# Performance work log

Measured on AMD Instinct MI355X. Metric: run time of the kernel, lower is better.

Reference implementation:

```python
import jax, jax.numpy as jnp
import numpy as np

B, N, E = 128, 2000, 2000
EMBED, HIDDEN = 256, 512


def setup_inputs() -> dict:
    key = jax.random.key(0)
    k1, k2, k3, k4, k5, k6, k7 = jax.random.split(key, 7)
    node_embeddings = jax.random.normal(k1, (B, N, EMBED), dtype=jnp.float32)
    locs = jax.random.uniform(k2, (B, N, 2), dtype=jnp.float32)
    edge_list = jax.random.randint(k3, (B, E, 2), 0, N, dtype=jnp.int64)
    in_dim = 2 * EMBED + 1
    # Kaiming-ish init for the two Linear layers of edge_scorer
    W1 = jax.random.normal(k4, (in_dim, HIDDEN), dtype=jnp.float32) / np.sqrt(in_dim)
    b1 = jnp.zeros((HIDDEN,), dtype=jnp.float32)
    W2 = jax.random.normal(k5, (HIDDEN, 1), dtype=jnp.float32) / np.sqrt(HIDDEN)
    b2 = jnp.zeros((1,), dtype=jnp.float32)
    return {
        "node_embeddings": node_embeddings,
        "locs": locs,
        "edge_list": edge_list,
        "delete_bias": 0,
        "W1": W1,
        "b1": b1,
        "W2": W2,
        "b2": b2,
    }


def reference(node_embeddings, locs, edge_list, delete_bias, W1, b1, W2, b2):
    # valid mask for -1-padded edges
    valid = (edge_list[..., 0] >= 0) & (edge_list[..., 1] >= 0)  # (B, E)
    edges = jnp.clip(edge_list, 0, None)
    bidx = jnp.arange(node_embeddings.shape[0])[:, None]  # (B, 1)
    i, j = edges[..., 0], edges[..., 1]  # (B, E)
    emb_i = node_embeddings[bidx, i]  # (B, E, D)
    emb_j = node_embeddings[bidx, j]  # (B, E, D)
    d = locs[bidx, i] - locs[bidx, j]  # (B, E, 2)
    dist = jnp.sqrt(jnp.sum(d * d, axis=-1, keepdims=True))  # (B, E, 1)
    feats = jnp.concatenate([emb_i, emb_j, dist], axis=-1)  # (B, E, 2D+1)
    h = jax.nn.relu(jnp.einsum('bef,fh->beh', feats, W1) + b1)
    logits = (jnp.einsum('beh,ho->beo', h, W2) + b2)[..., 0]  # (B, E)
    logits = jnp.where(valid, logits, -jnp.inf)
    return logits + jnp.float32(delete_bias)
```

## Files before the change

### kernel.cpp

```cpp
#include <hip/hip_runtime.h>
#include <math.h>

#define EMBED    256
#define HIDDEN   512
#define Nn       2000
#define Ee       2000
#define BM       128
#define TILES    8
#define NBLK     250
#define NTHREADS 512
#define FP       264

typedef __attribute__((ext_vector_type(8)))  short bf16x8;
typedef __attribute__((ext_vector_type(16))) float f32x16;

static __device__ __forceinline__ short f2bf(float f) {
  unsigned u = __builtin_bit_cast(unsigned, f);
  u += 0x7fffu + ((u >> 16) & 1u);
  return (short)(u >> 16);
}

static __device__ __forceinline__ bf16x8 cvt8(float4 a, float4 b) {
  bf16x8 v;
  v[0]=f2bf(a.x); v[1]=f2bf(a.y); v[2]=f2bf(a.z); v[3]=f2bf(a.w);
  v[4]=f2bf(b.x); v[5]=f2bf(b.y); v[6]=f2bf(b.z); v[7]=f2bf(b.w);
  return v;
}

#define LBAR() do { asm volatile("s_waitcnt lgkmcnt(0)" ::: "memory"); \
                    __builtin_amdgcn_s_barrier(); \
                    asm volatile("" ::: "memory"); } while (0)

__global__ void w1f_kernel(const float* __restrict__ W1, short* __restrict__ W1F) {
  const int t  = blockIdx.x * 512 + threadIdx.x;
  const int l  = t & 63;
  const int tk = (t >> 6) & 31;
  const int tn = t >> 11;
  const int n  = tn * 32 + (l & 31);
  const int k0 = tk * 16 + (l >> 5) * 8;
  bf16x8 v;
#pragma unroll
  for (int q = 0; q < 8; ++q)
    v[q] = f2bf(W1[(size_t)(k0 + q) * HIDDEN + n]);
  *(bf16x8*)(W1F + (size_t)t * 8) = v;
}

__global__ __launch_bounds__(NTHREADS, 2)
void edge_kernel(const float* __restrict__ emb, const float* __restrict__ locs,
                 const int* __restrict__ edges, const int* __restrict__ dbias,
                 const float* __restrict__ W1, const float* __restrict__ b1,
                 const float* __restrict__ W2, const float* __restrict__ b2,
                 const short* __restrict__ W1F, float* __restrict__ out)
{
  __shared__ short feat[2][BM][FP];
  __shared__ float b1_s[HIDDEN], w513_s[HIDDEN], w2_s[HIDDEN];
  __shared__ float part_s[8][BM];
  __shared__ float dist_s[2][BM];
  __shared__ int   valid_s[2][BM];
  __shared__ int   ibase_s[2][BM], jbase_s[2][BM];

  const int tid = threadIdx.x;

  const int orig = blockIdx.x;
  const int xcd  = orig & 7;
  const int idx  = orig >> 3;
  const int sbid = (xcd < 2 ? xcd * 32 : 64 + (xcd - 2) * 31) + idx;
  const int eblk = sbid * (TILES * BM);

  b1_s[tid]   = b1[tid];
  w513_s[tid] = W1[(size_t)512 * HIDDEN + tid];
  w2_s[tid]   = W2[tid];
  const float b2s_base = b2[0] + (float)dbias[0];

  auto do_meta = [&](int T) {
    const int g  = eblk + T * BM + tid;
    const int b  = g / Ee;
    const int i0 = edges[2 * g];
    const int j0 = edges[2 * g + 1];
    valid_s[T & 1][tid] = (i0 >= 0) && (j0 >= 0);
    const int ib = b * Nn + (i0 < 0 ? 0 : i0);
    const int jb = b * Nn + (j0 < 0 ? 0 : j0);
    ibase_s[T & 1][tid] = ib;
    jbase_s[T & 1][tid] = jb;
    const float dx = locs[2 * (size_t)ib]     - locs[2 * (size_t)jb];
    const float dy = locs[2 * (size_t)ib + 1] - locs[2 * (size_t)jb + 1];
    dist_s[T & 1][tid] = sqrtf(dx * dx + dy * dy);
  };

  if (tid < BM) do_meta(0);
  LBAR();

  const int sq = tid & 7;
  const int eh = tid >> 3;
  const int lane = tid & 63;
  const int w    = tid >> 6;
  const int ln31 = lane & 31;
  const int kg   = lane >> 5;

#pragma unroll
  for (int r = 0; r < 2; ++r) {
    const int el = r * 64 + eh;
    const float* src = emb + (size_t)ibase_s[0][el] * EMBED + sq * 8;
#pragma unroll
    for (int m = 0; m < 4; ++m) {
      float4 a  = *(const float4*)(src + m * 64);
      float4 b4 = *(const float4*)(src + m * 64 + 4);
      *(bf16x8*)&feat[0][el][(sq + 8 * m) * 8] = cvt8(a, b4);
    }
  }
  LBAR();

  f32x16 acc[4][2];
#pragma unroll
  for (int et = 0; et < 4; ++et)
#pragma unroll
    for (int nt = 0; nt < 2; ++nt)
#pragma unroll
      for (int q = 0; q < 16; ++q) acc[et][nt][q] = 0.f;

  const short* wfb = W1F + (size_t)(w * 2 * 32) * 512 + lane * 8;

#pragma unroll 1
  for (int p = 0; p < 2 * TILES; ++p) {
    const int bb   = p & 1;
    const int nbuf = bb ^ 1;
    const int half = p & 1;
    const int tps  = (p + 1) >> 1;
    const int sh   = (p + 1) & 1;
    const bool stg = p < 2 * TILES - 1;

    bf16x8 wc0 = *(const bf16x8*)(wfb + (size_t)(half * 16) * 512);
    bf16x8 wc1 = *(const bf16x8*)(wfb + (size_t)(32 + half * 16) * 512);

    float4 hg00, hg01, hg10, hg11;

#pragma unroll
    for (int ks = 0; ks < 16; ++ks) {
      bf16x8 wn0, wn1;
      if (ks < 15) {
        wn0 = *(const bf16x8*)(wfb + (size_t)(half * 16 + ks + 1) * 512);
        wn1 = *(const bf16x8*)(wfb + (size_t)(32 + half * 16 + ks + 1) * 512);
      }

      if (stg && (ks & 3) == 0) {
        const int g2 = ks >> 2;
        const int el = (g2 >> 1) * 64 + eh;
        const int rb = sh ? jbase_s[tps & 1][el] : ibase_s[tps & 1][el];
        const float* src = emb + (size_t)rb * EMBED + sq * 8 + (g2 & 1) * 128;
        hg00 = *(const float4*)(src);
        hg01 = *(const float4*)(src + 4);
        hg10 = *(const float4*)(src + 64);
        hg11 = *(const float4*)(src + 68);
      }
      if (stg && (ks & 3) == 3) {
        const int g2 = ks >> 2;
        const int el = (g2 >> 1) * 64 + eh;
        const int mb = (g2 & 1) * 2;
        *(bf16x8*)&feat[nbuf][el][(sq + 8 * mb) * 8]       = cvt8(hg00, hg01);
        *(bf16x8*)&feat[nbuf][el][(sq + 8 * (mb + 1)) * 8] = cvt8(hg10, hg11);
      }
      if ((p & 1) == 0 && ks == 1 && tid < BM && (p >> 1) + 1 < TILES)
        do_meta((p >> 1) + 1);

#pragma unroll
      for (int et = 0; et < 4; ++et) {
        bf16x8 fb = *(const bf16x8*)(&feat[bb][et * 32 + ln31][ks * 16 + kg * 8]);
        acc[et][0] = __builtin_amdgcn_mfma_f32_32x32x16_bf16(wc0, fb, acc[et][0], 0, 0, 0);
        acc[et][1] = __builtin_amdgcn_mfma_f32_32x32x16_bf16(wc1, fb, acc[et][1], 0, 0, 0);
      }
      wc0 = wn0; wc1 = wn1;
    }
    LBAR();

    if (p & 1) {
      const int t   = p >> 1;
      const int mb2 = t & 1;
      float dv[4], ps[4];
#pragma unroll
      for (int et = 0; et < 4; ++et) {
        dv[et] = dist_s[mb2][et * 32 + ln31];
        ps[et] = 0.f;
      }
#pragma unroll
      for (int nt = 0; nt < 2; ++nt) {
#pragma unroll
        for (int r = 0; r < 16; ++r) {
          const int n = w * 64 + nt * 32 + (r & 3) + ((r >> 2) << 3) + (kg << 2);
          const float bias = b1_s[n];
          const float wd   = w513_s[n];
          const float w2v  = w2_s[n];
#pragma unroll
          for (int et = 0; et < 4; ++et) {
            float pv = acc[et][nt][r] + bias + dv[et] * wd;
            ps[et] += fmaxf(pv, 0.f) * w2v;
          }
        }
      }
#pragma unroll
      for (int et = 0; et < 4; ++et) ps[et] += __shfl_xor(ps[et], 32, 64);
      if (lane < 32) {
#pragma unroll
        for (int et = 0; et < 4; ++et) part_s[w][et * 32 + ln31] = ps[et];
      }
      LBAR();
      if (tid < BM) {
        float s = 0.f;
#pragma unroll
        for (int wv = 0; wv < 8; ++wv) s += part_s[wv][tid];
        float logit = s + b2s_base;
        if (!valid_s[mb2][tid]) logit = -__builtin_inff();
        out[eblk + t * BM + tid] = logit;
      }
#pragma unroll
      for (int et = 0; et < 4; ++et)
#pragma unroll
        for (int nt = 0; nt < 2; ++nt)
#pragma unroll
          for (int q = 0; q < 16; ++q) acc[et][nt][q] = 0.f;
    }
  }
}

extern "C" void kernel_launch(void* const* d_in, const int* in_sizes, int n_in,
                              void* d_out, int out_size, void* d_ws, size_t ws_size,
                              hipStream_t stream) {
  const float* emb   = (const float*)d_in[0];
  const float* locs  = (const float*)d_in[1];
  const int*   edges = (const int*)d_in[2];
  const int*   dbias = (const int*)d_in[3];
  const float* W1    = (const float*)d_in[4];
  const float* b1    = (const float*)d_in[5];
  const float* W2    = (const float*)d_in[6];
  const float* b2    = (const float*)d_in[7];
  float*       out   = (float*)d_out;
  short*       W1F   = (short*)d_ws;

  w1f_kernel<<<dim3(64), dim3(512), 0, stream>>>(W1, W1F);
  edge_kernel<<<dim3(NBLK), dim3(NTHREADS), 0, stream>>>(
      emb, locs, edges, dbias, W1, b1, W2, b2, (const short*)W1F, out);
}
```

Measured before the change: 151.7 us.

## Repartition waves to 2 edge-halves by 4 hidden-groups and raise MFMA priority

The warp tiling changes from each wave covering all 128 edges by 64 hidden units to each wave covering 64 edges by 128 hidden units. Per k-step each wave now reads 2 feature fragments from LDS instead of 4, but loads 4 W1 fragments from global/L2 instead of 2. The goal is less LDS traffic per MFMA, at the cost of more global weight loads and extra weight registers. The MFMA block is also wrapped in s_setprio, and the cross-wave reduction is adjusted to the new layout.

```diff
diff --git a/kernel.cpp b/kernel.cpp
--- a/kernel.cpp
+++ b/kernel.cpp
@@ -54,7 +54,7 @@
 {
   __shared__ short feat[2][BM][FP];
   __shared__ float b1_s[HIDDEN], w513_s[HIDDEN], w2_s[HIDDEN];
-  __shared__ float part_s[8][BM];
+  __shared__ float part_s[8][64];
   __shared__ float dist_s[2][BM];
   __shared__ int   valid_s[2][BM];
   __shared__ int   ibase_s[2][BM], jbase_s[2][BM];
@@ -91,15 +91,17 @@
   LBAR();
 
   const int sq = tid & 7;
-  const int eh = tid >> 3;
+  const int ehs = tid >> 3;
   const int lane = tid & 63;
   const int w    = tid >> 6;
+  const int eh   = w & 1;
+  const int ng   = w >> 1;
   const int ln31 = lane & 31;
   const int kg   = lane >> 5;
 
 #pragma unroll
   for (int r = 0; r < 2; ++r) {
-    const int el = r * 64 + eh;
+    const int el = r * 64 + ehs;
     const float* src = emb + (size_t)ibase_s[0][el] * EMBED + sq * 8;
 #pragma unroll
     for (int m = 0; m < 4; ++m) {
@@ -110,15 +112,15 @@
   }
   LBAR();
 
-  f32x16 acc[4][2];
-#pragma unroll
-  for (int et = 0; et < 4; ++et)
-#pragma unroll
-    for (int nt = 0; nt < 2; ++nt)
+  f32x16 acc[2][4];
+#pragma unroll
+  for (int et = 0; et < 2; ++et)
+#pragma unroll
+    for (int nt = 0; nt < 4; ++nt)
 #pragma unroll
       for (int q = 0; q < 16; ++q) acc[et][nt][q] = 0.f;
 
-  const short* wfb = W1F + (size_t)(w * 2 * 32) * 512 + lane * 8;
+  const short* wfb = W1F + (size_t)(ng * 4 * 32) * 512 + lane * 8;
 
 #pragma unroll 1
   for (int p = 0; p < 2 * TILES; ++p) {
@@ -129,22 +131,24 @@
     const int sh   = (p + 1) & 1;
     const bool stg = p < 2 * TILES - 1;
 
-    bf16x8 wc0 = *(const bf16x8*)(wfb + (size_t)(half * 16) * 512);
-    bf16x8 wc1 = *(const bf16x8*)(wfb + (size_t)(32 + half * 16) * 512);
+    bf16x8 wc[4], wn[4];
+#pragma unroll
+    for (int nt = 0; nt < 4; ++nt)
+      wc[nt] = *(const bf16x8*)(wfb + (size_t)(nt * 32 + half * 16) * 512);
 
     float4 hg00, hg01, hg10, hg11;
 
 #pragma unroll
     for (int ks = 0; ks < 16; ++ks) {
-      bf16x8 wn0, wn1;
       if (ks < 15) {
-        wn0 = *(const bf16x8*)(wfb + (size_t)(half * 16 + ks + 1) * 512);
-        wn1 = *(const bf16x8*)(wfb + (size_t)(32 + half * 16 + ks + 1) * 512);
+#pragma unroll
+        for (int nt = 0; nt < 4; ++nt)
+          wn[nt] = *(const bf16x8*)(wfb + (size_t)(nt * 32 + half * 16 + ks + 1) * 512);
       }
 
       if (stg && (ks & 3) == 0) {
         const int g2 = ks >> 2;
-        const int el = (g2 >> 1) * 64 + eh;
+        const int el = (g2 >> 1) * 64 + ehs;
         const int rb = sh ? jbase_s[tps & 1][el] : ibase_s[tps & 1][el];
         const float* src = emb + (size_t)rb * EMBED + sq * 8 + (g2 & 1) * 128;
         hg00 = *(const float4*)(src);
@@ -154,7 +158,7 @@
       }
       if (stg && (ks & 3) == 3) {
         const int g2 = ks >> 2;
-        const int el = (g2 >> 1) * 64 + eh;
+        const int el = (g2 >> 1) * 64 + ehs;
         const int mb = (g2 & 1) * 2;
         *(bf16x8*)&feat[nbuf][el][(sq + 8 * mb) * 8]       = cvt8(hg00, hg01);
         *(bf16x8*)&feat[nbuf][el][(sq + 8 * (mb + 1)) * 8] = cvt8(hg10, hg11);
@@ -162,59 +166,65 @@
       if ((p & 1) == 0 && ks == 1 && tid < BM && (p >> 1) + 1 < TILES)
         do_meta((p >> 1) + 1);
 
-#pragma unroll
-      for (int et = 0; et < 4; ++et) {
-        bf16x8 fb = *(const bf16x8*)(&feat[bb][et * 32 + ln31][ks * 16 + kg * 8]);
-        acc[et][0] = __builtin_amdgcn_mfma_f32_32x32x16_bf16(wc0, fb, acc[et][0], 0, 0, 0);
-        acc[et][1] = __builtin_amdgcn_mfma_f32_32x32x16_bf16(wc1, fb, acc[et][1], 0, 0, 0);
-      }
-      wc0 = wn0; wc1 = wn1;
+      bf16x8 fb0 = *(const bf16x8*)(&feat[bb][eh * 64 + ln31][ks * 16 + kg * 8]);
+      bf16x8 fb1 = *(const bf16x8*)(&feat[bb][eh * 64 + 32 + ln31][ks * 16 + kg * 8]);
+
+      __builtin_amdgcn_s_setprio(1);
+#pragma unroll
+      for (int nt = 0; nt < 4; ++nt) {
+        acc[0][nt] = __builtin_amdgcn_mfma_f32_32x32x16_bf16(wc[nt], fb0, acc[0][nt], 0, 0, 0);
+        acc[1][nt] = __builtin_amdgcn_mfma_f32_32x32x16_bf16(wc[nt], fb1, acc[1][nt], 0, 0, 0);
+      }
+      __builtin_amdgcn_s_setprio(0);
+#pragma unroll
+      for (int nt = 0; nt < 4; ++nt) wc[nt] = wn[nt];
     }
     LBAR();
 
     if (p & 1) {
       const int t   = p >> 1;
       const int mb2 = t & 1;
-      float dv[4], ps[4];
-#pragma unroll
-      for (int et = 0; et < 4; ++et) {
-        dv[et] = dist_s[mb2][et * 32 + ln31];
+      float dv[2], ps[2];
+#pragma unroll
+      for (int et = 0; et < 2; ++et) {
+        dv[et] = dist_s[mb2][eh * 64 + et * 32 + ln31];
         ps[et] = 0.f;
       }
 #pragma unroll
-      for (int nt = 0; nt < 2; ++nt) {
+      for (int nt = 0; nt < 4; ++nt) {
 #pragma unroll
         for (int r = 0; r < 16; ++r) {
-          const int n = w * 64 + nt * 32 + (r & 3) + ((r >> 2) << 3) + (kg << 2);
+          const int n = ng * 128 + nt * 32 + (r & 3) + ((r >> 2) << 3) + (kg << 2);
           const float bias = b1_s[n];
           const float wd   = w513_s[n];
           const float w2v  = w2_s[n];
 #pragma unroll
-          for (int et = 0; et < 4; ++et) {
+          for (int et = 0; et < 2; ++et) {
             float pv = acc[et][nt][r] + bias + dv[et] * wd;
             ps[et] += fmaxf(pv, 0.f) * w2v;
           }
         }
       }
 #pragma unroll
-      for (int et = 0; et < 4; ++et) ps[et] += __shfl_xor(ps[et], 32, 64);
+      for (int et = 0; et < 2; ++et) ps[et] += __shfl_xor(ps[et], 32, 64);
       if (lane < 32) {
 #pragma unroll
-        for (int et = 0; et < 4; ++et) part_s[w][et * 32 + ln31] = ps[et];
+        for (int et = 0; et < 2; ++et) part_s[w][et * 32 + ln31] = ps[et];
       }
       LBAR();
       if (tid < BM) {
-        float s = 0.f;
-#pragma unroll
-        for (int wv = 0; wv < 8; ++wv) s += part_s[wv][tid];
+        const int ehh = tid >> 6;
+        const int es  = tid & 63;
+        float s = part_s[ehh][es] + part_s[2 + ehh][es] +
+                  part_s[4 + ehh][es] + part_s[6 + ehh][es];
         float logit = s + b2s_base;
         if (!valid_s[mb2][tid]) logit = -__builtin_inff();
         out[eblk + t * BM + tid] = logit;
       }
 #pragma unroll
-      for (int et = 0; et < 4; ++et)
-#pragma unroll
-        for (int nt = 0; nt < 2; ++nt)
+      for (int et = 0; et < 2; ++et)
+#pragma unroll
+        for (int nt = 0; nt < 4; ++nt)
 #pragma unroll
           for (int q = 0; q < 16; ++q) acc[et][nt][q] = 0.f;
     }
```

Result: slower. 162.8 us (+7.3%).

## Split edge kernel into producer and MFMA waves with smaller edge tiles

Applied to the files above, without the earlier changes.

Restructures the edge kernel around warp specialization. Four waves only issue MFMAs with raised priority and run the bias/ReLU/W2 epilogue. The other four waves gather and convert the next embedding tile, compute edge metadata and write the logits of the previous tile. The edge tile shrinks from 128 to 64 with twice as many tiles, and each MFMA wave now covers 256 hidden units for 32 edges. The goal is to hide gather latency behind compute and drop the extra in-loop barrier. The trade-off is half as many waves issuing MFMAs, and W1 fragments are now loaded from global memory inside the inner loop without the old register prefetch.

```diff
diff --git a/kernel.cpp b/kernel.cpp
--- a/kernel.cpp
+++ b/kernel.cpp
@@ -5,8 +5,8 @@
 #define HIDDEN   512
 #define Nn       2000
 #define Ee       2000
-#define BM       128
-#define TILES    8
+#define BM       64
+#define TILES    16
 #define NBLK     250
 #define NTHREADS 512
 #define FP       264
@@ -54,7 +54,7 @@
 {
   __shared__ short feat[2][BM][FP];
   __shared__ float b1_s[HIDDEN], w513_s[HIDDEN], w2_s[HIDDEN];
-  __shared__ float part_s[8][BM];
+  __shared__ float part_s[2][2][BM];
   __shared__ float dist_s[2][BM];
   __shared__ int   valid_s[2][BM];
   __shared__ int   ibase_s[2][BM], jbase_s[2][BM];
@@ -72,152 +72,121 @@
   w2_s[tid]   = W2[tid];
   const float b2s_base = b2[0] + (float)dbias[0];
 
-  auto do_meta = [&](int T) {
-    const int g  = eblk + T * BM + tid;
-    const int b  = g / Ee;
-    const int i0 = edges[2 * g];
-    const int j0 = edges[2 * g + 1];
-    valid_s[T & 1][tid] = (i0 >= 0) && (j0 >= 0);
-    const int ib = b * Nn + (i0 < 0 ? 0 : i0);
-    const int jb = b * Nn + (j0 < 0 ? 0 : j0);
-    ibase_s[T & 1][tid] = ib;
-    jbase_s[T & 1][tid] = jb;
-    const float dx = locs[2 * (size_t)ib]     - locs[2 * (size_t)jb];
-    const float dy = locs[2 * (size_t)ib + 1] - locs[2 * (size_t)jb + 1];
-    dist_s[T & 1][tid] = sqrtf(dx * dx + dy * dy);
-  };
-
-  if (tid < BM) do_meta(0);
-  LBAR();
-
-  const int sq = tid & 7;
-  const int eh = tid >> 3;
   const int lane = tid & 63;
   const int w    = tid >> 6;
   const int ln31 = lane & 31;
   const int kg   = lane >> 5;
 
-#pragma unroll
-  for (int r = 0; r < 2; ++r) {
-    const int el = r * 64 + eh;
-    const float* src = emb + (size_t)ibase_s[0][el] * EMBED + sq * 8;
-#pragma unroll
-    for (int m = 0; m < 4; ++m) {
-      float4 a  = *(const float4*)(src + m * 64);
-      float4 b4 = *(const float4*)(src + m * 64 + 4);
-      *(bf16x8*)&feat[0][el][(sq + 8 * m) * 8] = cvt8(a, b4);
+  const int pt  = tid - 256;
+  const int sq  = pt & 7;
+  const int ehs = (pt >> 3) & 31;
+
+  auto do_meta = [&](int T) {
+    const int g  = eblk + T * BM + pt;
+    const int b  = g / Ee;
+    const int i0 = edges[2 * g];
+    const int j0 = edges[2 * g + 1];
+    valid_s[T & 1][pt] = (i0 >= 0) && (j0 >= 0);
+    const int ib = b * Nn + (i0 < 0 ? 0 : i0);
+    const int jb = b * Nn + (j0 < 0 ? 0 : j0);
+    ibase_s[T & 1][pt] = ib;
+    jbase_s[T & 1][pt] = jb;
+    const float dx = locs[2 * (size_t)ib]     - locs[2 * (size_t)jb];
+    const float dy = locs[2 * (size_t)ib + 1] - locs[2 * (size_t)jb + 1];
+    dist_s[T & 1][pt] = sqrtf(dx * dx + dy * dy);
+  };
+
+  auto stage = [&](int tps, int sh, int dst) {
+#pragma unroll
+    for (int r = 0; r < 2; ++r) {
+      const int el = r * 32 + ehs;
+      const int rb = sh ? jbase_s[tps & 1][el] : ibase_s[tps & 1][el];
+      const float* src = emb + (size_t)rb * EMBED + sq * 8;
+#pragma unroll
+      for (int m = 0; m < 4; ++m) {
+        float4 a  = *(const float4*)(src + m * 64);
+        float4 b4 = *(const float4*)(src + m * 64 + 4);
+        *(bf16x8*)&feat[dst][el][(sq + 8 * m) * 8] = cvt8(a, b4);
+      }
     }
-  }
+  };
+
+  if (w == 4) do_meta(0);
   LBAR();
-
-  f32x16 acc[4][2];
-#pragma unroll
-  for (int et = 0; et < 4; ++et)
-#pragma unroll
-    for (int nt = 0; nt < 2; ++nt)
-#pragma unroll
-      for (int q = 0; q < 16; ++q) acc[et][nt][q] = 0.f;
-
-  const short* wfb = W1F + (size_t)(w * 2 * 32) * 512 + lane * 8;
+  if (w >= 4) stage(0, 0, 0);
+  LBAR();
+
+  const int eh = w & 1;
+  const int ng = w >> 1;
+
+  f32x16 acc[8];
+#pragma unroll
+  for (int nt = 0; nt < 8; ++nt)
+#pragma unroll
+    for (int q = 0; q < 16; ++q) acc[nt][q] = 0.f;
+
+  const short* wfb = W1F + (size_t)(ng * 8 * 32) * 512 + lane * 8;
 
 #pragma unroll 1
   for (int p = 0; p < 2 * TILES; ++p) {
     const int bb   = p & 1;
-    const int nbuf = bb ^ 1;
     const int half = p & 1;
-    const int tps  = (p + 1) >> 1;
-    const int sh   = (p + 1) & 1;
-    const bool stg = p < 2 * TILES - 1;
-
-    bf16x8 wc0 = *(const bf16x8*)(wfb + (size_t)(half * 16) * 512);
-    bf16x8 wc1 = *(const bf16x8*)(wfb + (size_t)(32 + half * 16) * 512);
-
-    float4 hg00, hg01, hg10, hg11;
-
-#pragma unroll
-    for (int ks = 0; ks < 16; ++ks) {
-      bf16x8 wn0, wn1;
-      if (ks < 15) {
-        wn0 = *(const bf16x8*)(wfb + (size_t)(half * 16 + ks + 1) * 512);
-        wn1 = *(const bf16x8*)(wfb + (size_t)(32 + half * 16 + ks + 1) * 512);
-      }
-
-      if (stg && (ks & 3) == 0) {
-        const int g2 = ks >> 2;
-        const int el = (g2 >> 1) * 64 + eh;
-        const int rb = sh ? jbase_s[tps & 1][el] : ibase_s[tps & 1][el];
-        const float* src = emb + (size_t)rb * EMBED + sq * 8 + (g2 & 1) * 128;
-        hg00 = *(const float4*)(src);
-        hg01 = *(const float4*)(src + 4);
-        hg10 = *(const float4*)(src + 64);
-        hg11 = *(const float4*)(src + 68);
-      }
-      if (stg && (ks & 3) == 3) {
-        const int g2 = ks >> 2;
-        const int el = (g2 >> 1) * 64 + eh;
-        const int mb = (g2 & 1) * 2;
-        *(bf16x8*)&feat[nbuf][el][(sq + 8 * mb) * 8]       = cvt8(hg00, hg01);
-        *(bf16x8*)&feat[nbuf][el][(sq + 8 * (mb + 1)) * 8] = cvt8(hg10, hg11);
-      }
-      if ((p & 1) == 0 && ks == 1 && tid < BM && (p >> 1) + 1 < TILES)
-        do_meta((p >> 1) + 1);
-
-#pragma unroll
-      for (int et = 0; et < 4; ++et) {
-        bf16x8 fb = *(const bf16x8*)(&feat[bb][et * 32 + ln31][ks * 16 + kg * 8]);
-        acc[et][0] = __builtin_amdgcn_mfma_f32_32x32x16_bf16(wc0, fb, acc[et][0], 0, 0, 0);
-        acc[et][1] = __builtin_amdgcn_mfma_f32_32x32x16_bf16(wc1, fb, acc[et][1], 0, 0, 0);
-      }
-      wc0 = wn0; wc1 = wn1;
+
+    if (w < 4) {
+      __builtin_amdgcn_s_setprio(1);
+#pragma unroll
+      for (int ks = 0; ks < 16; ++ks) {
+        bf16x8 fb = *(const bf16x8*)(&feat[bb][eh * 32 + ln31][ks * 16 + kg * 8]);
+#pragma unroll
+        for (int nt = 0; nt < 8; ++nt) {
+          bf16x8 wa = *(const bf16x8*)(wfb + (size_t)(nt * 32 + half * 16 + ks) * 512);
+          acc[nt] = __builtin_amdgcn_mfma_f32_32x32x16_bf16(wa, fb, acc[nt], 0, 0, 0);
+        }
+      }
+      __builtin_amdgcn_s_setprio(0);
+
+      if (p & 1) {
+        const int t   = p >> 1;
+        const int par = t & 1;
+        const float dv = dist_s[par][eh * 32 + ln31];
+        float ps = 0.f;
+#pragma unroll
+        for (int nt = 0; nt < 8; ++nt) {
+#pragma unroll
+          for (int r = 0; r < 16; ++r) {
+            const int n = ng * 256 + nt * 32 + (r & 3) + ((r >> 2) << 3) + (kg << 2);
+            float pv = acc[nt][r] + b1_s[n] + dv * w513_s[n];
+            ps += fmaxf(pv, 0.f) * w2_s[n];
+          }
+        }
+        ps += __shfl_xor(ps, 32, 64);
+        if (lane < 32) part_s[par][ng][eh * 32 + ln31] = ps;
+#pragma unroll
+        for (int nt = 0; nt < 8; ++nt)
+#pragma unroll
+          for (int q = 0; q < 16; ++q) acc[nt][q] = 0.f;
+      }
+    } else {
+      if (p < 2 * TILES - 1)
+        stage((p + 1) >> 1, (p + 1) & 1, (p + 1) & 1);
+      if (!(p & 1)) {
+        const int t = p >> 1;
+        if (t >= 1 && pt < BM) {
+          const int par = (t - 1) & 1;
+          float s = part_s[par][0][pt] + part_s[par][1][pt] + b2s_base;
+          if (!valid_s[par][pt]) s = -__builtin_inff();
+          out[eblk + (t - 1) * BM + pt] = s;
+        }
+        if (w == 4 && t + 1 < TILES) do_meta(t + 1);
+      }
     }
     LBAR();
-
-    if (p & 1) {
-      const int t   = p >> 1;
-      const int mb2 = t & 1;
-      float dv[4], ps[4];
-#pragma unroll
-      for (int et = 0; et < 4; ++et) {
-        dv[et] = dist_s[mb2][et * 32 + ln31];
-        ps[et] = 0.f;
-      }
-#pragma unroll
-      for (int nt = 0; nt < 2; ++nt) {
-#pragma unroll
-        for (int r = 0; r < 16; ++r) {
-          const int n = w * 64 + nt * 32 + (r & 3) + ((r >> 2) << 3) + (kg << 2);
-          const float bias = b1_s[n];
-          const float wd   = w513_s[n];
-          const float w2v  = w2_s[n];
-#pragma unroll
-          for (int et = 0; et < 4; ++et) {
-            float pv = acc[et][nt][r] + bias + dv[et] * wd;
-            ps[et] += fmaxf(pv, 0.f) * w2v;
-          }
-        }
-      }
-#pragma unroll
-      for (int et = 0; et < 4; ++et) ps[et] += __shfl_xor(ps[et], 32, 64);
-      if (lane < 32) {
-#pragma unroll
-        for (int et = 0; et < 4; ++et) part_s[w][et * 32 + ln31] = ps[et];
-      }
-      LBAR();
-      if (tid < BM) {
-        float s = 0.f;
-#pragma unroll
-        for (int wv = 0; wv < 8; ++wv) s += part_s[wv][tid];
-        float logit = s + b2s_base;
-        if (!valid_s[mb2][tid]) logit = -__builtin_inff();
-        out[eblk + t * BM + tid] = logit;
-      }
-#pragma unroll
-      for (int et = 0; et < 4; ++et)
-#pragma unroll
-        for (int nt = 0; nt < 2; ++nt)
-#pragma unroll
-          for (int q = 0; q < 16; ++q) acc[et][nt][q] = 0.f;
-    }
+  }
+
+  if (tid < BM) {
+    float s = part_s[1][0][tid] + part_s[1][1][tid] + b2s_base;
+    if (!valid_s[1][tid]) s = -__builtin_inff();
+    out[eblk + (TILES - 1) * BM + tid] = s;
   }
 }
 
```

After: 505.8 us. +233.4%, slower.

## Stage W1 weight chunks through LDS in finer K-phases with double-buffered features

Applied to the files above, without the earlier changes.

Splits each edge tile's K=512 reduction into eight 64-wide phases. Each phase cooperatively loads a 64-K slice of the pre-swizzled bf16 W1 into shared memory and gathers the matching embedding slice into a smaller feature buffer, instead of each wave streaming W1 fragments directly from global memory. The next phase's weights and gathers are prefetched into registers while the current phase's MFMAs run, and s_setprio is raised around the MFMA block. The aim is to replace redundant per-wave global W1 reads with shared reuse and to shrink LDS for features. The cost is a 64 KB weight buffer, two barriers per phase, and four times as many loop iterations.

```diff
diff --git a/kernel.cpp b/kernel.cpp
--- a/kernel.cpp
+++ b/kernel.cpp
@@ -9,7 +9,7 @@
 #define TILES    8
 #define NBLK     250
 #define NTHREADS 512
-#define FP       264
+#define FP       72
 
 typedef __attribute__((ext_vector_type(8)))  short bf16x8;
 typedef __attribute__((ext_vector_type(16))) float f32x16;
@@ -52,6 +52,7 @@
                  const float* __restrict__ W2, const float* __restrict__ b2,
                  const short* __restrict__ W1F, float* __restrict__ out)
 {
+  __shared__ short wlds[64 * 512];
   __shared__ short feat[2][BM][FP];
   __shared__ float b1_s[HIDDEN], w513_s[HIDDEN], w2_s[HIDDEN];
   __shared__ float part_s[8][BM];
@@ -87,26 +88,35 @@
     dist_s[T & 1][tid] = sqrtf(dx * dx + dy * dy);
   };
 
-  if (tid < BM) do_meta(0);
-  LBAR();
-
-  const int sq = tid & 7;
-  const int eh = tid >> 3;
+  const int sub = tid & 7;
+  const int grp = tid >> 3;
+  const int e   = tid >> 2;
+  const int sq  = tid & 3;
+
   const int lane = tid & 63;
   const int w    = tid >> 6;
   const int ln31 = lane & 31;
   const int kg   = lane >> 5;
 
-#pragma unroll
-  for (int r = 0; r < 2; ++r) {
-    const int el = r * 64 + eh;
-    const float* src = emb + (size_t)ibase_s[0][el] * EMBED + sq * 8;
-#pragma unroll
-    for (int m = 0; m < 4; ++m) {
-      float4 a  = *(const float4*)(src + m * 64);
-      float4 b4 = *(const float4*)(src + m * 64 + 4);
-      *(bf16x8*)&feat[0][el][(sq + 8 * m) * 8] = cvt8(a, b4);
-    }
+  if (tid < BM) do_meta(0);
+  LBAR();
+
+  {
+    const int F = (grp >> 2) * 32 + (grp & 3);
+    bf16x8 wr[8];
+#pragma unroll
+    for (int i = 0; i < 8; ++i)
+      wr[i] = *(const bf16x8*)(W1F + (size_t)F * 512 + (sub + 8 * i) * 8);
+    const float* src = emb + (size_t)ibase_s[0][e] * EMBED + sq * 16;
+    float4 g0 = *(const float4*)(src);
+    float4 g1 = *(const float4*)(src + 4);
+    float4 g2 = *(const float4*)(src + 8);
+    float4 g3 = *(const float4*)(src + 12);
+#pragma unroll
+    for (int i = 0; i < 8; ++i)
+      *(bf16x8*)&wlds[grp * 512 + (sub + 8 * i) * 8] = wr[i];
+    *(bf16x8*)&feat[0][e][sq * 16]     = cvt8(g0, g1);
+    *(bf16x8*)&feat[0][e][sq * 16 + 8] = cvt8(g2, g3);
   }
   LBAR();
 
@@ -118,67 +128,70 @@
 #pragma unroll
       for (int q = 0; q < 16; ++q) acc[et][nt][q] = 0.f;
 
-  const short* wfb = W1F + (size_t)(w * 2 * 32) * 512 + lane * 8;
+  const int waoff0 = ((w * 2 + 0) * 4) * 512 + lane * 8;
+  const int waoff1 = ((w * 2 + 1) * 4) * 512 + lane * 8;
 
 #pragma unroll 1
-  for (int p = 0; p < 2 * TILES; ++p) {
+  for (int p = 0; p < 8 * TILES; ++p) {
+    const int tile = p >> 3;
+    const int ph8  = p & 7;
     const int bb   = p & 1;
-    const int nbuf = bb ^ 1;
-    const int half = p & 1;
-    const int tps  = (p + 1) >> 1;
-    const int sh   = (p + 1) & 1;
-    const bool stg = p < 2 * TILES - 1;
-
-    bf16x8 wc0 = *(const bf16x8*)(wfb + (size_t)(half * 16) * 512);
-    bf16x8 wc1 = *(const bf16x8*)(wfb + (size_t)(32 + half * 16) * 512);
-
-    float4 hg00, hg01, hg10, hg11;
-
-#pragma unroll
-    for (int ks = 0; ks < 16; ++ks) {
-      bf16x8 wn0, wn1;
-      if (ks < 15) {
-        wn0 = *(const bf16x8*)(wfb + (size_t)(half * 16 + ks + 1) * 512);
-        wn1 = *(const bf16x8*)(wfb + (size_t)(32 + half * 16 + ks + 1) * 512);
-      }
-
-      if (stg && (ks & 3) == 0) {
-        const int g2 = ks >> 2;
-        const int el = (g2 >> 1) * 64 + eh;
-        const int rb = sh ? jbase_s[tps & 1][el] : ibase_s[tps & 1][el];
-        const float* src = emb + (size_t)rb * EMBED + sq * 8 + (g2 & 1) * 128;
-        hg00 = *(const float4*)(src);
-        hg01 = *(const float4*)(src + 4);
-        hg10 = *(const float4*)(src + 64);
-        hg11 = *(const float4*)(src + 68);
-      }
-      if (stg && (ks & 3) == 3) {
-        const int g2 = ks >> 2;
-        const int el = (g2 >> 1) * 64 + eh;
-        const int mb = (g2 & 1) * 2;
-        *(bf16x8*)&feat[nbuf][el][(sq + 8 * mb) * 8]       = cvt8(hg00, hg01);
-        *(bf16x8*)&feat[nbuf][el][(sq + 8 * (mb + 1)) * 8] = cvt8(hg10, hg11);
-      }
-      if ((p & 1) == 0 && ks == 1 && tid < BM && (p >> 1) + 1 < TILES)
-        do_meta((p >> 1) + 1);
-
+    const int nb   = bb ^ 1;
+    const bool more = (p < 8 * TILES - 1);
+
+    bf16x8 wr[8];
+    float4 gr0, gr1, gr2, gr3;
+    if (more) {
+      const int pn   = p + 1;
+      const int ph8n = pn & 7;
+      const int sn   = ph8n >> 2;
+      const int qn   = ph8n & 3;
+      const int tn_  = pn >> 3;
+      const int F = (grp >> 2) * 32 + sn * 16 + qn * 4 + (grp & 3);
+#pragma unroll
+      for (int i = 0; i < 8; ++i)
+        wr[i] = *(const bf16x8*)(W1F + (size_t)F * 512 + (sub + 8 * i) * 8);
+      const int* mb = sn ? jbase_s[tn_ & 1] : ibase_s[tn_ & 1];
+      const float* src = emb + (size_t)mb[e] * EMBED + qn * 64 + sq * 16;
+      gr0 = *(const float4*)(src);
+      gr1 = *(const float4*)(src + 4);
+      gr2 = *(const float4*)(src + 8);
+      gr3 = *(const float4*)(src + 12);
+    }
+
+#pragma unroll
+    for (int ks = 0; ks < 4; ++ks) {
+      bf16x8 wa0 = *(const bf16x8*)&wlds[waoff0 + ks * 512];
+      bf16x8 wa1 = *(const bf16x8*)&wlds[waoff1 + ks * 512];
+      __builtin_amdgcn_s_setprio(1);
 #pragma unroll
       for (int et = 0; et < 4; ++et) {
         bf16x8 fb = *(const bf16x8*)(&feat[bb][et * 32 + ln31][ks * 16 + kg * 8]);
-        acc[et][0] = __builtin_amdgcn_mfma_f32_32x32x16_bf16(wc0, fb, acc[et][0], 0, 0, 0);
-        acc[et][1] = __builtin_amdgcn_mfma_f32_32x32x16_bf16(wc1, fb, acc[et][1], 0, 0, 0);
-      }
-      wc0 = wn0; wc1 = wn1;
-    }
+        acc[et][0] = __builtin_amdgcn_mfma_f32_32x32x16_bf16(wa0, fb, acc[et][0], 0, 0, 0);
+        acc[et][1] = __builtin_amdgcn_mfma_f32_32x32x16_bf16(wa1, fb, acc[et][1], 0, 0, 0);
+      }
+      __builtin_amdgcn_s_setprio(0);
+    }
+
+    if (ph8 == 0 && tile + 1 < TILES && tid < BM) do_meta(tile + 1);
+
     LBAR();
 
-    if (p & 1) {
-      const int t   = p >> 1;
-      const int mb2 = t & 1;
+    if (more) {
+#pragma unroll
+      for (int i = 0; i < 8; ++i)
+        *(bf16x8*)&wlds[grp * 512 + (sub + 8 * i) * 8] = wr[i];
+      *(bf16x8*)&feat[nb][e][sq * 16]     = cvt8(gr0, gr1);
+      *(bf16x8*)&feat[nb][e][sq * 16 + 8] = cvt8(gr2, gr3);
+    }
+    LBAR();
+
+    if (ph8 == 7) {
+      const int par = tile & 1;
       float dv[4], ps[4];
 #pragma unroll
       for (int et = 0; et < 4; ++et) {
-        dv[et] = dist_s[mb2][et * 32 + ln31];
+        dv[et] = dist_s[par][et * 32 + ln31];
         ps[et] = 0.f;
       }
 #pragma unroll
@@ -208,8 +221,8 @@
 #pragma unroll
         for (int wv = 0; wv < 8; ++wv) s += part_s[wv][tid];
         float logit = s + b2s_base;
-        if (!valid_s[mb2][tid]) logit = -__builtin_inff();
-        out[eblk + t * BM + tid] = logit;
+        if (!valid_s[par][tid]) logit = -__builtin_inff();
+        out[eblk + tile * BM + tid] = logit;
       }
 #pragma unroll
       for (int et = 0; et < 4; ++et)
```

Result: slower. 176.3 us (+16.2%).
